# Performance work log

Hardware: AMD Instinct MI355X
Metric: run time of the kernel (lower is better)

The kernel has to match this reference:

```python
import jax, jax.numpy as jnp
import numpy as np
import math

B, S, K, H, NH = 4, 1024, 512, 1024, 16
HD = H // NH  # 64


def _split_heads(x):
    # [B, L, H] -> [B, NH, L, HD]
    b, l, _ = x.shape
    return x.reshape(b, l, NH, HD).transpose(0, 2, 1, 3)


def setup_inputs() -> dict:
    key = jax.random.key(0)
    ks = jax.random.split(key, 16)
    scale = 1.0 / math.sqrt(H)
    d = {
        'hidden_states': jax.random.normal(ks[0], (B, S, H), jnp.float32),
        'encoder_hidden_states': jax.random.normal(ks[1], (B, K, H), jnp.float32),
        'attention_mask': jnp.zeros((B, 1, 1, S), jnp.float32),
        'encoder_attention_mask': jnp.zeros((B, 1, 1, K), jnp.float32),
    }
    names = ['q', 'k', 'v', 'kq', 'kk', 'kv']
    for i, n in enumerate(names):
        d[f'W{n}'] = jax.random.normal(ks[2 + i], (H, H), jnp.float32) * scale
        d[f'b{n}'] = jnp.zeros((H,), jnp.float32)
    return d


def reference(hidden_states, encoder_hidden_states, attention_mask, encoder_attention_mask,
              Wq, bq, Wk, bk, Wv, bv, Wkq, bkq, Wkk, bkk, Wkv, bkv):
    inv = 1.0 / math.sqrt(HD)
    # self branch
    q = _split_heads(hidden_states @ Wq + bq)            # [B,NH,S,HD]
    k = _split_heads(hidden_states @ Wk + bk)
    v = _split_heads(hidden_states @ Wv + bv)
    scores = jnp.einsum('bhsd,bhtd->bhst', q, k) * inv + attention_mask
    probs = jax.nn.softmax(scores, axis=-1)              # [B,NH,S,S]
    ctx = jnp.einsum('bhst,bhtd->bhsd', probs, v)
    # knowledge branch
    kq = _split_heads(hidden_states @ Wkq + bkq)          # [B,NH,S,HD]
    kk = _split_heads(encoder_hidden_states @ Wkk + bkk)  # [B,NH,K,HD]
    kv = _split_heads(encoder_hidden_states @ Wkv + bkv)
    kscores = jnp.einsum('bhsd,bhtd->bhst', kq, kk) * inv + encoder_attention_mask
    kprobs = jax.nn.softmax(kscores, axis=-1)            # [B,NH,S,K]
    kctx = jnp.einsum('bhst,bhtd->bhsd', kprobs, kv)
    # merge heads and average branches
    out = (ctx + kctx) * 0.5                             # [B,NH,S,HD]
    out = out.transpose(0, 2, 1, 3).reshape(B, S, H)
    return out
```

## Files before the change

### kernel.cpp

```cpp
#include <hip/hip_runtime.h>

#define BATCH 4
#define SEQ   1024
#define KENC  512
#define HDIM  1024
#define NHEAD 16
#define HD    64
#define LOG2E 1.44269504088896340736f

typedef __attribute__((ext_vector_type(8))) short bf16x8;
typedef __attribute__((ext_vector_type(4))) float f32x4;
typedef __attribute__((ext_vector_type(16))) float f32x16;
typedef __attribute__((ext_vector_type(4))) float f4v;
typedef __attribute__((ext_vector_type(4))) short s4v;

__device__ __forceinline__ short f2bf(float f) {
  unsigned u = __float_as_uint(f);
  u += 0x7fffu + ((u >> 16) & 1u);
  return (short)(u >> 16);
}

__device__ __forceinline__ void gload_lds16(const void* g, void* l) {
  __builtin_amdgcn_global_load_lds(
      (const __attribute__((address_space(1))) void*)g,
      (__attribute__((address_space(3))) void*)l, 16, 0, 0);
}

#define MF(A, B, C) __builtin_amdgcn_mfma_f32_16x16x32_bf16((A), (B), (C), 0, 0, 0)

__global__ __launch_bounds__(256) void cast2(const float* __restrict__ sa,
                                             short* __restrict__ da, int n4a,
                                             const float* __restrict__ sb,
                                             short* __restrict__ db, int n4b) {
  int i = blockIdx.x * 256 + threadIdx.x;
  const float* s;
  short* d;
  int j;
  if (i < n4a) { s = sa; d = da; j = i; }
  else { j = i - n4a; if (j >= n4b) return; s = sb; d = db; }
  f4v v = ((const f4v*)s)[j];
  s4v o;
#pragma unroll
  for (int k = 0; k < 4; ++k) o[k] = f2bf(v[k]);
  ((s4v*)d)[j] = o;
}

struct WtArgs { const float* W[6]; };

__global__ __launch_bounds__(256) void wt_cast(WtArgs a, short* __restrict__ wt) {
  int j = blockIdx.z;
  const float* W = a.W[j];
  short* dst = wt + (size_t)j * (HDIM * HDIM);
  int cb = blockIdx.x * 32, rb = blockIdx.y * 32;
  __shared__ float t[32][33];
  int tx = threadIdx.x & 31, ty = threadIdx.x >> 5;
#pragma unroll
  for (int rr = 0; rr < 4; ++rr)
    t[ty + rr * 8][tx] = W[(size_t)(rb + ty + rr * 8) * HDIM + cb + tx];
  __syncthreads();
#pragma unroll
  for (int rr = 0; rr < 4; ++rr)
    dst[(size_t)(cb + ty + rr * 8) * HDIM + rb + tx] = f2bf(t[tx][ty + rr * 8]);
}

struct ProjArgs {
  const short* X[6];
  const short* Wt[6];
  const float* bias[6];
  short* out[6];
  int tshift[6];
  int mode[6];
  float scale[6];
};

__global__ __launch_bounds__(256) void proj_gemm(ProjArgs a) {
  int lid = blockIdx.x;
  int t = (lid & 7) * 160 + (lid >> 3);
  int job, bx, by;
  if (t < 1024) { job = t >> 8; int r = t & 255; bx = r & 7; by = r >> 3; }
  else { int u = t - 1024; job = 4 + (u >> 7); int r = u & 127; bx = r & 7; by = r >> 3; }

  const short* X = a.X[job];
  const short* W = a.Wt[job];

  __shared__ __align__(16) char Lds[65536];

  int tid = threadIdx.x, lane = tid & 63, wave = tid >> 6;
  int wr = wave >> 1, wc = wave & 1;
  int l15 = lane & 15, g4 = lane >> 4;

  f32x4 acc[4][4];
#pragma unroll
  for (int m = 0; m < 4; ++m)
#pragma unroll
    for (int n = 0; n < 4; ++n)
#pragma unroll
      for (int r = 0; r < 4; ++r) acc[m][n][r] = 0.0f;

  int arow = by * 128, brow = bx * 128;
  const int crow = lane >> 2;
  const int sgrp = (lane & 3) ^ ((lane >> 2) & 3) ^ (lane >> 4);
  const int rsw = (lane & 3) ^ (l15 >> 2);

  const char* Xb = (const char*)X;
  const char* Wb = (const char*)W;
  const size_t sac0 = ((size_t)(arow + 32 * wave + crow) * HDIM + sgrp * 8) * 2;
  const size_t sac1 = sac0 + (size_t)16 * HDIM * 2;
  const size_t sbc0 = ((size_t)(brow + 32 * wave + crow) * HDIM + sgrp * 8) * 2;
  const size_t sbc1 = sbc0 + (size_t)16 * HDIM * 2;
  const int ldA0 = wave * 2048, ldA1 = ldA0 + 1024;
  const int ldB0 = 8192 + ldA0, ldB1 = ldB0 + 1024;

  const int aoff = wr * 4096 + l15 * 64 + ((g4 ^ rsw) << 4);
  const int boff = 8192 + wc * 4096 + l15 * 64 + ((g4 ^ rsw) << 4);

#define STG_A(SBO, SKT)                                                  \
  do {                                                                   \
    gload_lds16(Xb + sac0 + (size_t)(SKT) * 64, Lds + (SBO) + ldA0);     \
    gload_lds16(Xb + sac1 + (size_t)(SKT) * 64, Lds + (SBO) + ldA1);     \
  } while (0)
#define STG_B(SBO, SKT)                                                  \
  do {                                                                   \
    gload_lds16(Wb + sbc0 + (size_t)(SKT) * 64, Lds + (SBO) + ldB0);     \
    gload_lds16(Wb + sbc1 + (size_t)(SKT) * 64, Lds + (SBO) + ldB1);     \
  } while (0)

  STG_A(0, 0);     STG_B(0, 0);
  STG_A(16384, 1); STG_B(16384, 1);
  STG_A(32768, 2); STG_B(32768, 2);
  asm volatile("s_waitcnt vmcnt(8)" ::: "memory");
  __builtin_amdgcn_s_barrier();
  asm volatile("" ::: "memory");

#define STEP(BO, DO_STG, SBO, SKT, VMW, ENDBAR)                               \
  do {                                                                        \
                   \
    bf16x8 a0 = *(const bf16x8*)(Lds + (BO) + 0 * 1024 + aoff);               \
    bf16x8 a1 = *(const bf16x8*)(Lds + (BO) + 1 * 1024 + aoff);               \
    bf16x8 b0 = *(const bf16x8*)(Lds + (BO) + 0 * 1024 + boff);               \
    bf16x8 b1 = *(const bf16x8*)(Lds + (BO) + 1 * 1024 + boff);               \
    bf16x8 b2 = *(const bf16x8*)(Lds + (BO) + 2 * 1024 + boff);               \
    bf16x8 b3 = *(const bf16x8*)(Lds + (BO) + 3 * 1024 + boff);               \
    if (DO_STG) STG_A(SBO, SKT);                                              \
    __builtin_amdgcn_sched_barrier(0);                                        \
    __builtin_amdgcn_s_barrier();                                             \
    asm volatile("s_waitcnt lgkmcnt(0)" ::: "memory");                        \
    __builtin_amdgcn_sched_barrier(0);                                        \
    __builtin_amdgcn_s_setprio(1);                                            \
    acc[0][0] = MF(a0, b0, acc[0][0]);                                        \
    acc[0][1] = MF(a0, b1, acc[0][1]);                                        \
    acc[0][2] = MF(a0, b2, acc[0][2]);                                        \
    acc[0][3] = MF(a0, b3, acc[0][3]);                                        \
    acc[1][0] = MF(a1, b0, acc[1][0]);                                        \
    acc[1][1] = MF(a1, b1, acc[1][1]);                                        \
    acc[1][2] = MF(a1, b2, acc[1][2]);                                        \
    acc[1][3] = MF(a1, b3, acc[1][3]);                                        \
    __builtin_amdgcn_s_setprio(0);                                            \
    __builtin_amdgcn_sched_barrier(0);                                        \
    __builtin_amdgcn_s_barrier();                                             \
                    \
    bf16x8 a2 = *(const bf16x8*)(Lds + (BO) + 2 * 1024 + aoff);               \
    bf16x8 a3 = *(const bf16x8*)(Lds + (BO) + 3 * 1024 + aoff);               \
    if (DO_STG) STG_B(SBO, SKT);                                              \
    __builtin_amdgcn_sched_barrier(0);                                        \
    __builtin_amdgcn_s_barrier();                                             \
    asm volatile("s_waitcnt lgkmcnt(0)" ::: "memory");                        \
    __builtin_amdgcn_sched_barrier(0);                                        \
    __builtin_amdgcn_s_setprio(1);                                            \
    acc[2][0] = MF(a2, b0, acc[2][0]);                                        \
    acc[2][1] = MF(a2, b1, acc[2][1]);                                        \
    acc[2][2] = MF(a2, b2, acc[2][2]);                                        \
    acc[2][3] = MF(a2, b3, acc[2][3]);                                        \
    acc[3][0] = MF(a3, b0, acc[3][0]);                                        \
    acc[3][1] = MF(a3, b1, acc[3][1]);                                        \
    acc[3][2] = MF(a3, b2, acc[3][2]);                                        \
    acc[3][3] = MF(a3, b3, acc[3][3]);                                        \
    __builtin_amdgcn_s_setprio(0);                                            \
    asm volatile(VMW ::: "memory");                                           \
    __builtin_amdgcn_sched_barrier(0);                                        \
    if (ENDBAR) {                                                             \
      __builtin_amdgcn_s_barrier();                                           \
      asm volatile("" ::: "memory");                                          \
    }                                                                         \
  } while (0)

#pragma unroll 1
  for (int tt = 0; tt < 29; ++tt) {
    int bo = (tt & 3) << 14;
    int sbo = ((tt + 3) & 3) << 14;
    STEP(bo, 1, sbo, tt + 3, "s_waitcnt vmcnt(8)", 1);
  }
  STEP((29 & 3) << 14, 0, 0, 0, "s_waitcnt vmcnt(4)", 1);
  STEP((30 & 3) << 14, 0, 0, 0, "s_waitcnt vmcnt(0)", 1);
  STEP((31 & 3) << 14, 0, 0, 0, "s_nop 0", 0);

#undef STEP
#undef STG_A
#undef STG_B

  const float* bias = a.bias[job];
  short* out = a.out[job];
  int tshift = a.tshift[job], tmask = (1 << tshift) - 1, mode = a.mode[job];
  float scl = a.scale[job];
#pragma unroll
  for (int m = 0; m < 4; ++m) {
    int rowb = arow + wr * 64 + m * 16 + (g4 << 2);
#pragma unroll
    for (int n = 0; n < 4; ++n) {
      int col = brow + wc * 64 + n * 16 + l15;
      float bv = bias[col];
      int head = col >> 6, d = col & 63;
#pragma unroll
      for (int r = 0; r < 4; ++r) {
        int row = rowb + r;
        int bb = row >> tshift, tk = row & tmask;
        float val = (acc[m][n][r] + bv) * scl;
        size_t idx;
        if (mode == 0)
          idx = ((((size_t)bb * NHEAD + head) << tshift) + tk) * 64 + d;
        else
          idx = ((((size_t)bb * NHEAD + head) * 64 + d) << tshift) + tk;
        out[idx] = f2bf(val);
      }
    }
  }
}

__global__ __launch_bounds__(256, 3) void attn32(
    const short* __restrict__ qall, const short* __restrict__ kall,
    const short* __restrict__ vTall, const short* __restrict__ kqall,
    const short* __restrict__ kkall, const short* __restrict__ kvTall,
    const float* __restrict__ amask, const float* __restrict__ emask,
    float* __restrict__ out) {
  __shared__ char KT[2][8192];
  __shared__ char VT[2][8192];
  __shared__ float red[4][32];

  int lid = blockIdx.x;
  int id = (lid & 7) * 64 + (lid >> 3);
  int bh = id >> 3, qb = id & 7;
  int b = bh >> 4, h = bh & 15;
  int lane = threadIdx.x & 63, wave = threadIdx.x >> 6;
  int l31 = lane & 31, hi = lane >> 5, x7 = l31 & 7;
  int qrow0 = qb * 128 + wave * 32;

  bf16x8 qcur[4];
  {
    const short* qp = qall + ((size_t)bh * SEQ + qrow0 + l31) * 64;
#pragma unroll
    for (int i = 0; i < 4; ++i)
      qcur[i] = *(const bf16x8*)(qp + i * 16 + hi * 8);
  }

  const char* kb0 = (const char*)(kall + (size_t)bh * SEQ * 64);
  const char* vb0 = (const char*)(vTall + (size_t)bh * 64 * SEQ);
  const char* kb1 = (const char*)(kkall + (size_t)bh * KENC * 64);
  const char* vb1 = (const char*)(kvTall + (size_t)bh * 64 * KENC);
  const float* mpc = amask + (size_t)b * SEQ;

  auto STAGE = [&](int pb, const char* kb, const char* vb, size_t vrowb, int kt) {
    int t0 = threadIdx.x;
#pragma unroll
    for (int c = 0; c < 2; ++c) {
      int idx = c * 256 + t0;
      int row = idx >> 3, phys = idx & 7;
      int lg = phys ^ (row & 7);
      gload_lds16(kb + ((size_t)(kt * 64 + row)) * 128 + lg * 16,
                  KT[pb] + idx * 16);
      gload_lds16(vb + (size_t)row * vrowb + (size_t)kt * 128 + lg * 16,
                  VT[pb] + idx * 16);
    }
  };

  STAGE(0, kb0, vb0, SEQ * 2, 0);

  f32x16 ctx0, ctx1, c10, c11;
#pragma unroll
  for (int r = 0; r < 16; ++r) { ctx0[r] = 0.f; ctx1[r] = 0.f; c10[r] = 0.f; c11[r] = 0.f; }
  float mr = -1e30f, lr = 0.f;

#pragma unroll 1
  for (int t = 0; t < 24; ++t) {
    int p = t & 1;
    __syncthreads();
    if (t < 23) {
      int tn = t + 1;
      if (tn >= 16) STAGE(p ^ 1, kb1, vb1, KENC * 2, tn - 16);
      else          STAGE(p ^ 1, kb0, vb0, SEQ * 2, tn);
    }
    if (t == 16) {
      if (!hi) red[wave][l31] = lr;
      asm volatile("s_waitcnt lgkmcnt(0)" ::: "memory");
#pragma unroll
      for (int r2 = 0; r2 < 4; ++r2) {
        f4v lv = *(const f4v*)(&red[wave][r2 * 8 + 4 * hi]);
#pragma unroll
        for (int j2 = 0; j2 < 4; ++j2) {
          float li = __builtin_amdgcn_rcpf(lv[j2]);
          int r = r2 * 4 + j2;
          c10[r] = ctx0[r] * li;  ctx0[r] = 0.f;
          c11[r] = ctx1[r] * li;  ctx1[r] = 0.f;
        }
      }
      mr = -1e30f; lr = 0.f;
      const short* kqp = kqall + ((size_t)bh * SEQ + qrow0 + l31) * 64;
#pragma unroll
      for (int i = 0; i < 4; ++i)
        qcur[i] = *(const bf16x8*)(kqp + i * 16 + hi * 8);
      mpc = emask + (size_t)b * KENC;
    }
    int kt = (t >= 16) ? t - 16 : t;
    const char* Kp = KT[p];
    const char* Vp = VT[p];

    f32x16 s0, s1;
#pragma unroll
    for (int r = 0; r < 16; ++r) { s0[r] = 0.f; s1[r] = 0.f; }
    __builtin_amdgcn_s_setprio(1);
#pragma unroll
    for (int i = 0; i < 4; ++i) {
      bf16x8 kf = *(const bf16x8*)(Kp + (l31)*128 + (((2 * i + hi) ^ x7) << 4));
      s0 = __builtin_amdgcn_mfma_f32_32x32x16_bf16(kf, qcur[i], s0, 0, 0, 0);
    }
#pragma unroll
    for (int i = 0; i < 4; ++i) {
      bf16x8 kf = *(const bf16x8*)(Kp + (32 + l31) * 128 + (((2 * i + hi) ^ x7) << 4));
      s1 = __builtin_amdgcn_mfma_f32_32x32x16_bf16(kf, qcur[i], s1, 0, 0, 0);
    }
    __builtin_amdgcn_s_setprio(0);

    const float* mp = mpc + kt * 64;
#pragma unroll
    for (int r2 = 0; r2 < 4; ++r2) {
      f4v ma = *(const f4v*)(mp + r2 * 8 + 4 * hi);
      f4v mb = *(const f4v*)(mp + 32 + r2 * 8 + 4 * hi);
#pragma unroll
      for (int j2 = 0; j2 < 4; ++j2) {
        s0[r2 * 4 + j2] = fmaf(ma[j2], LOG2E, s0[r2 * 4 + j2]);
        s1[r2 * 4 + j2] = fmaf(mb[j2], LOG2E, s1[r2 * 4 + j2]);
      }
    }

    float mx = s0[0];
#pragma unroll
    for (int r = 1; r < 16; ++r) mx = fmaxf(mx, s0[r]);
#pragma unroll
    for (int r = 0; r < 16; ++r) mx = fmaxf(mx, s1[r]);
    mx = fmaxf(mx, __int_as_float(__shfl_xor(__float_as_int(mx), 32)));

    if (!__all(mx <= mr + 12.f)) {
      float mn = fmaxf(mr, mx);
      float scl = __builtin_amdgcn_exp2f(mr - mn);
      mr = mn; lr *= scl;
      if (!hi) red[wave][l31] = scl;
      asm volatile("s_waitcnt lgkmcnt(0)" ::: "memory");
#pragma unroll
      for (int r2 = 0; r2 < 4; ++r2) {
        f4v sv = *(const f4v*)(&red[wave][r2 * 8 + 4 * hi]);
#pragma unroll
        for (int j2 = 0; j2 < 4; ++j2) {
          ctx0[r2 * 4 + j2] *= sv[j2];
          ctx1[r2 * 4 + j2] *= sv[j2];
        }
      }
    }

    float rs = 0.f;
#pragma unroll
    for (int r = 0; r < 16; ++r) { s0[r] = __builtin_amdgcn_exp2f(s0[r] - mr); rs += s0[r]; }
#pragma unroll
    for (int r = 0; r < 16; ++r) { s1[r] = __builtin_amdgcn_exp2f(s1[r] - mr); rs += s1[r]; }
    rs += __int_as_float(__shfl_xor(__float_as_int(rs), 32));
    lr += rs;

#pragma unroll
    for (int s = 0; s < 2; ++s) {
      const f32x16& sv = s ? s1 : s0;
      unsigned W[8];
#pragma unroll
      for (int r2 = 0; r2 < 4; ++r2) {
        asm("v_cvt_pk_bf16_f32 %0, %1, %2"
            : "=v"(W[r2 * 2]) : "v"(sv[r2 * 4 + 0]), "v"(sv[r2 * 4 + 1]));
        asm("v_cvt_pk_bf16_f32 %0, %1, %2"
            : "=v"(W[r2 * 2 + 1]) : "v"(sv[r2 * 4 + 2]), "v"(sv[r2 * 4 + 3]));
      }
#pragma unroll
      for (int jr = 0; jr < 2; ++jr) {
        unsigned sendA = hi ? W[(2 * jr) * 2]     : W[(2 * jr + 1) * 2];
        unsigned sendB = hi ? W[(2 * jr) * 2 + 1] : W[(2 * jr + 1) * 2 + 1];
        unsigned rA = (unsigned)__shfl_xor((int)sendA, 32);
        unsigned rB = (unsigned)__shfl_xor((int)sendB, 32);
        union { unsigned u[4]; bf16x8 v; } pa;
        if (!hi) { pa.u[0] = W[2 * jr * 2]; pa.u[1] = W[2 * jr * 2 + 1];
                   pa.u[2] = rA;            pa.u[3] = rB; }
        else     { pa.u[0] = rA;            pa.u[1] = rB;
                   pa.u[2] = W[(2 * jr + 1) * 2]; pa.u[3] = W[(2 * jr + 1) * 2 + 1]; }
        int j = s * 2 + jr;
        __builtin_amdgcn_s_setprio(1);
        bf16x8 vf0 = *(const bf16x8*)(Vp + (l31)*128 + (((2 * j + hi) ^ x7) << 4));
        ctx0 = __builtin_amdgcn_mfma_f32_32x32x16_bf16(pa.v, vf0, ctx0, 0, 0, 0);
        bf16x8 vf1 = *(const bf16x8*)(Vp + (32 + l31) * 128 + (((2 * j + hi) ^ x7) << 4));
        ctx1 = __builtin_amdgcn_mfma_f32_32x32x16_bf16(pa.v, vf1, ctx1, 0, 0, 0);
        __builtin_amdgcn_s_setprio(0);
      }
    }
  }

  if (!hi) red[wave][l31] = lr;
  asm volatile("s_waitcnt lgkmcnt(0)" ::: "memory");
  float* op = out + ((size_t)b * SEQ) * HDIM + h * 64 + l31;
#pragma unroll
  for (int r2 = 0; r2 < 4; ++r2) {
    f4v lv = *(const f4v*)(&red[wave][r2 * 8 + 4 * hi]);
#pragma unroll
    for (int j2 = 0; j2 < 4; ++j2) {
      float li = __builtin_amdgcn_rcpf(lv[j2]);
      int s = qrow0 + r2 * 8 + 4 * hi + j2;
      int r = r2 * 4 + j2;
      op[(size_t)s * HDIM]      = 0.5f * (c10[r] + ctx0[r] * li);
      op[(size_t)s * HDIM + 32] = 0.5f * (c11[r] + ctx1[r] * li);
    }
  }
}

extern "C" void kernel_launch(void* const* d_in, const int* in_sizes, int n_in,
                              void* d_out, int out_size, void* d_ws, size_t ws_size,
                              hipStream_t stream) {
  const float* hid = (const float*)d_in[0];
  const float* enc = (const float*)d_in[1];
  const float* amask = (const float*)d_in[2];
  const float* emask = (const float*)d_in[3];

  char* ws = (char*)d_ws;
  short* hbf = (short*)(ws);
  short* ebf = (short*)(ws + (8u << 20));
  short* wt = (short*)(ws + (12u << 20));
  short* qo = (short*)(ws + (24u << 20));
  short* ko = (short*)(ws + (32u << 20));
  short* vT = (short*)(ws + (40u << 20));
  short* kqo = (short*)(ws + (48u << 20));
  short* kko = (short*)(ws + (56u << 20));
  short* kvT = (short*)(ws + (60u << 20));

  cast2<<<6144, 256, 0, stream>>>(hid, hbf, (BATCH * SEQ * HDIM) / 4,
                                  enc, ebf, (BATCH * KENC * HDIM) / 4);

  WtArgs wa;
  for (int j = 0; j < 6; ++j) wa.W[j] = (const float*)d_in[4 + 2 * j];
  wt_cast<<<dim3(32, 32, 6), 256, 0, stream>>>(wa, wt);

  ProjArgs pa;
  const short* Xs[6] = {hbf, hbf, hbf, hbf, ebf, ebf};
  short* outs[6] = {qo, ko, vT, kqo, kko, kvT};
  const int tsh[6] = {10, 10, 10, 10, 9, 9};
  const int md[6] = {0, 0, 1, 0, 0, 1};
  const float qscale = 0.125f * LOG2E;
  const float scl[6] = {qscale, 1.f, 1.f, qscale, 1.f, 1.f};
  for (int j = 0; j < 6; ++j) {
    pa.X[j] = Xs[j];
    pa.Wt[j] = wt + (size_t)j * (HDIM * HDIM);
    pa.bias[j] = (const float*)d_in[5 + 2 * j];
    pa.out[j] = outs[j];
    pa.tshift[j] = tsh[j];
    pa.mode[j] = md[j];
    pa.scale[j] = scl[j];
  }
  proj_gemm<<<1280, 256, 0, stream>>>(pa);

  attn32<<<512, 256, 0, stream>>>(qo, ko, vT, kqo, kko, kvT, amask, emask,
                                  (float*)d_out);
}
```

Baseline: 151.1 us.

## Pair projection GEMMs sharing the same input to reuse A tiles

Projections that read the same activation (q/k, v/kq, kk/kv) are merged into one block that computes two output tiles, so each A tile is loaded once and reused against two weight tiles. The pipeline becomes a three-stage LDS ring of 24 KB per stage, and the mid-step barriers and split loads are removed. The grid is halved to 640 blocks. Each block now holds 128 accumulator floats per thread, which raises register pressure and may lower occupancy or cause spills. It also relies on 72 KB of shared memory per block.

```diff
diff --git a/kernel.cpp b/kernel.cpp
--- a/kernel.cpp
+++ b/kernel.cpp
@@ -64,7 +64,7 @@
 }
 
 struct ProjArgs {
-  const short* X[6];
+  const short* X[3];
   const short* Wt[6];
   const float* bias[6];
   short* out[6];
@@ -73,29 +73,29 @@
   float scale[6];
 };
 
-__global__ __launch_bounds__(256) void proj_gemm(ProjArgs a) {
+__global__ __launch_bounds__(256) void proj_pair(ProjArgs a) {
   int lid = blockIdx.x;
-  int t = (lid & 7) * 160 + (lid >> 3);
-  int job, bx, by;
-  if (t < 1024) { job = t >> 8; int r = t & 255; bx = r & 7; by = r >> 3; }
-  else { int u = t - 1024; job = 4 + (u >> 7); int r = u & 127; bx = r & 7; by = r >> 3; }
-
-  const short* X = a.X[job];
-  const short* W = a.Wt[job];
-
-  __shared__ __align__(16) char Lds[65536];
+  int pair, bx, by;
+  if (lid < 512) { pair = lid >> 8; int r = lid & 255; bx = r & 7; by = r >> 3; }
+  else           { pair = 2; int r = lid - 512;        bx = r & 7; by = r >> 3; }
+
+  const short* X = a.X[pair];
+  const char* W0b = (const char*)a.Wt[pair * 2];
+  const char* W1b = (const char*)a.Wt[pair * 2 + 1];
+
+  __shared__ __align__(16) char Lds[3 * 24576];
 
   int tid = threadIdx.x, lane = tid & 63, wave = tid >> 6;
   int wr = wave >> 1, wc = wave & 1;
   int l15 = lane & 15, g4 = lane >> 4;
 
-  f32x4 acc[4][4];
+  f32x4 acc0[4][4], acc1[4][4];
 #pragma unroll
   for (int m = 0; m < 4; ++m)
 #pragma unroll
     for (int n = 0; n < 4; ++n)
 #pragma unroll
-      for (int r = 0; r < 4; ++r) acc[m][n][r] = 0.0f;
+      for (int r = 0; r < 4; ++r) { acc0[m][n][r] = 0.0f; acc1[m][n][r] = 0.0f; }
 
   int arow = by * 128, brow = bx * 128;
   const int crow = lane >> 2;
@@ -103,81 +103,90 @@
   const int rsw = (lane & 3) ^ (l15 >> 2);
 
   const char* Xb = (const char*)X;
-  const char* Wb = (const char*)W;
-  const size_t sac0 = ((size_t)(arow + 32 * wave + crow) * HDIM + sgrp * 8) * 2;
-  const size_t sac1 = sac0 + (size_t)16 * HDIM * 2;
-  const size_t sbc0 = ((size_t)(brow + 32 * wave + crow) * HDIM + sgrp * 8) * 2;
-  const size_t sbc1 = sbc0 + (size_t)16 * HDIM * 2;
+  const size_t sa0 = ((size_t)(arow + 32 * wave + crow) * HDIM + sgrp * 8) * 2;
+  const size_t sa1 = sa0 + (size_t)16 * HDIM * 2;
+  const size_t sb0 = ((size_t)(brow + 32 * wave + crow) * HDIM + sgrp * 8) * 2;
+  const size_t sb1 = sb0 + (size_t)16 * HDIM * 2;
   const int ldA0 = wave * 2048, ldA1 = ldA0 + 1024;
-  const int ldB0 = 8192 + ldA0, ldB1 = ldB0 + 1024;
 
   const int aoff = wr * 4096 + l15 * 64 + ((g4 ^ rsw) << 4);
-  const int boff = 8192 + wc * 4096 + l15 * 64 + ((g4 ^ rsw) << 4);
-
-#define STG_A(SBO, SKT)                                                  \
-  do {                                                                   \
-    gload_lds16(Xb + sac0 + (size_t)(SKT) * 64, Lds + (SBO) + ldA0);     \
-    gload_lds16(Xb + sac1 + (size_t)(SKT) * 64, Lds + (SBO) + ldA1);     \
+  const int boff = wc * 4096 + l15 * 64 + ((g4 ^ rsw) << 4);
+
+#define STG_A(SBO, SKT)                                                      \
+  do {                                                                       \
+    gload_lds16(Xb + sa0 + (size_t)(SKT) * 64, Lds + (SBO) + ldA0);          \
+    gload_lds16(Xb + sa1 + (size_t)(SKT) * 64, Lds + (SBO) + ldA1);          \
   } while (0)
-#define STG_B(SBO, SKT)                                                  \
-  do {                                                                   \
-    gload_lds16(Wb + sbc0 + (size_t)(SKT) * 64, Lds + (SBO) + ldB0);     \
-    gload_lds16(Wb + sbc1 + (size_t)(SKT) * 64, Lds + (SBO) + ldB1);     \
+#define STG_B0(SBO, SKT)                                                     \
+  do {                                                                       \
+    gload_lds16(W0b + sb0 + (size_t)(SKT) * 64, Lds + (SBO) + 8192 + ldA0);  \
+    gload_lds16(W0b + sb1 + (size_t)(SKT) * 64, Lds + (SBO) + 8192 + ldA1);  \
   } while (0)
-
-  STG_A(0, 0);     STG_B(0, 0);
-  STG_A(16384, 1); STG_B(16384, 1);
-  STG_A(32768, 2); STG_B(32768, 2);
-  asm volatile("s_waitcnt vmcnt(8)" ::: "memory");
+#define STG_B1(SBO, SKT)                                                     \
+  do {                                                                       \
+    gload_lds16(W1b + sb0 + (size_t)(SKT) * 64, Lds + (SBO) + 16384 + ldA0); \
+    gload_lds16(W1b + sb1 + (size_t)(SKT) * 64, Lds + (SBO) + 16384 + ldA1); \
+  } while (0)
+
+  STG_A(0, 0);     STG_B0(0, 0);     STG_B1(0, 0);
+  STG_A(24576, 1); STG_B0(24576, 1); STG_B1(24576, 1);
+  asm volatile("s_waitcnt vmcnt(6)" ::: "memory");
   __builtin_amdgcn_s_barrier();
   asm volatile("" ::: "memory");
 
 #define STEP(BO, DO_STG, SBO, SKT, VMW, ENDBAR)                               \
   do {                                                                        \
-                   \
     bf16x8 a0 = *(const bf16x8*)(Lds + (BO) + 0 * 1024 + aoff);               \
     bf16x8 a1 = *(const bf16x8*)(Lds + (BO) + 1 * 1024 + aoff);               \
-    bf16x8 b0 = *(const bf16x8*)(Lds + (BO) + 0 * 1024 + boff);               \
-    bf16x8 b1 = *(const bf16x8*)(Lds + (BO) + 1 * 1024 + boff);               \
-    bf16x8 b2 = *(const bf16x8*)(Lds + (BO) + 2 * 1024 + boff);               \
-    bf16x8 b3 = *(const bf16x8*)(Lds + (BO) + 3 * 1024 + boff);               \
-    if (DO_STG) STG_A(SBO, SKT);                                              \
-    __builtin_amdgcn_sched_barrier(0);                                        \
-    __builtin_amdgcn_s_barrier();                                             \
-    asm volatile("s_waitcnt lgkmcnt(0)" ::: "memory");                        \
-    __builtin_amdgcn_sched_barrier(0);                                        \
-    __builtin_amdgcn_s_setprio(1);                                            \
-    acc[0][0] = MF(a0, b0, acc[0][0]);                                        \
-    acc[0][1] = MF(a0, b1, acc[0][1]);                                        \
-    acc[0][2] = MF(a0, b2, acc[0][2]);                                        \
-    acc[0][3] = MF(a0, b3, acc[0][3]);                                        \
-    acc[1][0] = MF(a1, b0, acc[1][0]);                                        \
-    acc[1][1] = MF(a1, b1, acc[1][1]);                                        \
-    acc[1][2] = MF(a1, b2, acc[1][2]);                                        \
-    acc[1][3] = MF(a1, b3, acc[1][3]);                                        \
-    __builtin_amdgcn_s_setprio(0);                                            \
-    __builtin_amdgcn_sched_barrier(0);                                        \
-    __builtin_amdgcn_s_barrier();                                             \
-                    \
     bf16x8 a2 = *(const bf16x8*)(Lds + (BO) + 2 * 1024 + aoff);               \
     bf16x8 a3 = *(const bf16x8*)(Lds + (BO) + 3 * 1024 + aoff);               \
-    if (DO_STG) STG_B(SBO, SKT);                                              \
-    __builtin_amdgcn_sched_barrier(0);                                        \
-    __builtin_amdgcn_s_barrier();                                             \
-    asm volatile("s_waitcnt lgkmcnt(0)" ::: "memory");                        \
-    __builtin_amdgcn_sched_barrier(0);                                        \
+    bf16x8 p0 = *(const bf16x8*)(Lds + (BO) + 8192 + 0 * 1024 + boff);        \
+    bf16x8 p1 = *(const bf16x8*)(Lds + (BO) + 8192 + 1 * 1024 + boff);        \
+    bf16x8 p2 = *(const bf16x8*)(Lds + (BO) + 8192 + 2 * 1024 + boff);        \
+    bf16x8 p3 = *(const bf16x8*)(Lds + (BO) + 8192 + 3 * 1024 + boff);        \
+    bf16x8 q0 = *(const bf16x8*)(Lds + (BO) + 16384 + 0 * 1024 + boff);       \
+    bf16x8 q1 = *(const bf16x8*)(Lds + (BO) + 16384 + 1 * 1024 + boff);       \
+    bf16x8 q2 = *(const bf16x8*)(Lds + (BO) + 16384 + 2 * 1024 + boff);       \
+    bf16x8 q3 = *(const bf16x8*)(Lds + (BO) + 16384 + 3 * 1024 + boff);       \
+    if (DO_STG) { STG_A(SBO, SKT); STG_B0(SBO, SKT); }                        \
     __builtin_amdgcn_s_setprio(1);                                            \
-    acc[2][0] = MF(a2, b0, acc[2][0]);                                        \
-    acc[2][1] = MF(a2, b1, acc[2][1]);                                        \
-    acc[2][2] = MF(a2, b2, acc[2][2]);                                        \
-    acc[2][3] = MF(a2, b3, acc[2][3]);                                        \
-    acc[3][0] = MF(a3, b0, acc[3][0]);                                        \
-    acc[3][1] = MF(a3, b1, acc[3][1]);                                        \
-    acc[3][2] = MF(a3, b2, acc[3][2]);                                        \
-    acc[3][3] = MF(a3, b3, acc[3][3]);                                        \
+    acc0[0][0] = MF(a0, p0, acc0[0][0]);                                      \
+    acc0[0][1] = MF(a0, p1, acc0[0][1]);                                      \
+    acc0[0][2] = MF(a0, p2, acc0[0][2]);                                      \
+    acc0[0][3] = MF(a0, p3, acc0[0][3]);                                      \
+    acc0[1][0] = MF(a1, p0, acc0[1][0]);                                      \
+    acc0[1][1] = MF(a1, p1, acc0[1][1]);                                      \
+    acc0[1][2] = MF(a1, p2, acc0[1][2]);                                      \
+    acc0[1][3] = MF(a1, p3, acc0[1][3]);                                      \
+    acc0[2][0] = MF(a2, p0, acc0[2][0]);                                      \
+    acc0[2][1] = MF(a2, p1, acc0[2][1]);                                      \
+    acc0[2][2] = MF(a2, p2, acc0[2][2]);                                      \
+    acc0[2][3] = MF(a2, p3, acc0[2][3]);                                      \
+    acc0[3][0] = MF(a3, p0, acc0[3][0]);                                      \
+    acc0[3][1] = MF(a3, p1, acc0[3][1]);                                      \
+    acc0[3][2] = MF(a3, p2, acc0[3][2]);                                      \
+    acc0[3][3] = MF(a3, p3, acc0[3][3]);                                      \
+    __builtin_amdgcn_s_setprio(0);                                            \
+    if (DO_STG) STG_B1(SBO, SKT);                                             \
+    __builtin_amdgcn_s_setprio(1);                                            \
+    acc1[0][0] = MF(a0, q0, acc1[0][0]);                                      \
+    acc1[0][1] = MF(a0, q1, acc1[0][1]);                                      \
+    acc1[0][2] = MF(a0, q2, acc1[0][2]);                                      \
+    acc1[0][3] = MF(a0, q3, acc1[0][3]);                                      \
+    acc1[1][0] = MF(a1, q0, acc1[1][0]);                                      \
+    acc1[1][1] = MF(a1, q1, acc1[1][1]);                                      \
+    acc1[1][2] = MF(a1, q2, acc1[1][2]);                                      \
+    acc1[1][3] = MF(a1, q3, acc1[1][3]);                                      \
+    acc1[2][0] = MF(a2, q0, acc1[2][0]);                                      \
+    acc1[2][1] = MF(a2, q1, acc1[2][1]);                                      \
+    acc1[2][2] = MF(a2, q2, acc1[2][2]);                                      \
+    acc1[2][3] = MF(a2, q3, acc1[2][3]);                                      \
+    acc1[3][0] = MF(a3, q0, acc1[3][0]);                                      \
+    acc1[3][1] = MF(a3, q1, acc1[3][1]);                                      \
+    acc1[3][2] = MF(a3, q2, acc1[3][2]);                                      \
+    acc1[3][3] = MF(a3, q3, acc1[3][3]);                                      \
     __builtin_amdgcn_s_setprio(0);                                            \
     asm volatile(VMW ::: "memory");                                           \
-    __builtin_amdgcn_sched_barrier(0);                                        \
     if (ENDBAR) {                                                             \
       __builtin_amdgcn_s_barrier();                                           \
       asm volatile("" ::: "memory");                                          \
@@ -185,42 +194,48 @@
   } while (0)
 
 #pragma unroll 1
-  for (int tt = 0; tt < 29; ++tt) {
-    int bo = (tt & 3) << 14;
-    int sbo = ((tt + 3) & 3) << 14;
-    STEP(bo, 1, sbo, tt + 3, "s_waitcnt vmcnt(8)", 1);
-  }
-  STEP((29 & 3) << 14, 0, 0, 0, "s_waitcnt vmcnt(4)", 1);
-  STEP((30 & 3) << 14, 0, 0, 0, "s_waitcnt vmcnt(0)", 1);
-  STEP((31 & 3) << 14, 0, 0, 0, "s_nop 0", 0);
+  for (int it = 0; it < 10; ++it) {
+    int t0 = it * 3;
+    STEP(0,     1, 49152, t0 + 2, "s_waitcnt vmcnt(6)", 1);
+    STEP(24576, 1, 0,     t0 + 3, "s_waitcnt vmcnt(6)", 1);
+    STEP(49152, 1, 24576, t0 + 4, "s_waitcnt vmcnt(6)", 1);
+  }
+  STEP(0,     0, 0, 0, "s_waitcnt vmcnt(0)", 1);
+  STEP(24576, 0, 0, 0, "s_nop 0", 0);
 
 #undef STEP
 #undef STG_A
-#undef STG_B
-
-  const float* bias = a.bias[job];
-  short* out = a.out[job];
-  int tshift = a.tshift[job], tmask = (1 << tshift) - 1, mode = a.mode[job];
-  float scl = a.scale[job];
-#pragma unroll
-  for (int m = 0; m < 4; ++m) {
-    int rowb = arow + wr * 64 + m * 16 + (g4 << 2);
-#pragma unroll
-    for (int n = 0; n < 4; ++n) {
-      int col = brow + wc * 64 + n * 16 + l15;
-      float bv = bias[col];
-      int head = col >> 6, d = col & 63;
-#pragma unroll
-      for (int r = 0; r < 4; ++r) {
-        int row = rowb + r;
-        int bb = row >> tshift, tk = row & tmask;
-        float val = (acc[m][n][r] + bv) * scl;
-        size_t idx;
-        if (mode == 0)
-          idx = ((((size_t)bb * NHEAD + head) << tshift) + tk) * 64 + d;
-        else
-          idx = ((((size_t)bb * NHEAD + head) * 64 + d) << tshift) + tk;
-        out[idx] = f2bf(val);
+#undef STG_B0
+#undef STG_B1
+
+#pragma unroll
+  for (int jj = 0; jj < 2; ++jj) {
+    int j = pair * 2 + jj;
+    const float* bias = a.bias[j];
+    short* out = a.out[j];
+    int tshift = a.tshift[j], tmask = (1 << tshift) - 1, mode = a.mode[j];
+    float scl = a.scale[j];
+#pragma unroll
+    for (int m = 0; m < 4; ++m) {
+      int rowb = arow + wr * 64 + m * 16 + (g4 << 2);
+#pragma unroll
+      for (int n = 0; n < 4; ++n) {
+        int col = brow + wc * 64 + n * 16 + l15;
+        float bv = bias[col];
+        int head = col >> 6, d = col & 63;
+#pragma unroll
+        for (int r = 0; r < 4; ++r) {
+          int row = rowb + r;
+          int bb = row >> tshift, tk = row & tmask;
+          float v = jj ? acc1[m][n][r] : acc0[m][n][r];
+          float val = (v + bv) * scl;
+          size_t idx;
+          if (mode == 0)
+            idx = ((((size_t)bb * NHEAD + head) << tshift) + tk) * 64 + d;
+          else
+            idx = ((((size_t)bb * NHEAD + head) * 64 + d) << tshift) + tk;
+          out[idx] = f2bf(val);
+        }
       }
     }
   }
@@ -450,14 +465,13 @@
   wt_cast<<<dim3(32, 32, 6), 256, 0, stream>>>(wa, wt);
 
   ProjArgs pa;
-  const short* Xs[6] = {hbf, hbf, hbf, hbf, ebf, ebf};
+  pa.X[0] = hbf; pa.X[1] = hbf; pa.X[2] = ebf;
   short* outs[6] = {qo, ko, vT, kqo, kko, kvT};
   const int tsh[6] = {10, 10, 10, 10, 9, 9};
   const int md[6] = {0, 0, 1, 0, 0, 1};
   const float qscale = 0.125f * LOG2E;
   const float scl[6] = {qscale, 1.f, 1.f, qscale, 1.f, 1.f};
   for (int j = 0; j < 6; ++j) {
-    pa.X[j] = Xs[j];
     pa.Wt[j] = wt + (size_t)j * (HDIM * HDIM);
     pa.bias[j] = (const float*)d_in[5 + 2 * j];
     pa.out[j] = outs[j];
@@ -465,7 +479,7 @@
     pa.mode[j] = md[j];
     pa.scale[j] = scl[j];
   }
-  proj_gemm<<<1280, 256, 0, stream>>>(pa);
+  proj_pair<<<640, 256, 0, stream>>>(pa);
 
   attn32<<<512, 256, 0, stream>>>(qo, ko, vT, kqo, kko, kvT, amask, emask,
                                   (float*)d_out);
```

Measured after the change: 166.7 us. 1.1x slower.
